# Optimization experiments

Hardware: AMD Instinct MI355X
Metric: run time of the kernel (lower is better)

## Reference

```python
import jax, jax.numpy as jnp
import numpy as np

D_MODEL = 1024
NUM_HEADS = 16
D_K = D_MODEL // NUM_HEADS


def setup_inputs() -> dict:
    key = jax.random.key(0)
    ks = jax.random.split(key, 9)
    B, S = 2, 2048
    s = 1.0 / np.sqrt(D_MODEL)
    inp = {
        "x": jax.random.normal(ks[0], (B, S, D_MODEL), dtype=jnp.float32),
        "Wq": jax.random.normal(ks[1], (D_MODEL, D_MODEL), dtype=jnp.float32) * s,
        "bq": jnp.zeros((D_MODEL,), dtype=jnp.float32),
        "Wk": jax.random.normal(ks[2], (D_MODEL, D_MODEL), dtype=jnp.float32) * s,
        "bk": jnp.zeros((D_MODEL,), dtype=jnp.float32),
        "Wv": jax.random.normal(ks[3], (D_MODEL, D_MODEL), dtype=jnp.float32) * s,
        "bv": jnp.zeros((D_MODEL,), dtype=jnp.float32),
        "Wo": jax.random.normal(ks[4], (D_MODEL, D_MODEL), dtype=jnp.float32) * s,
        "bo": jnpp if False else jnp.zeros((D_MODEL,), dtype=jnp.float32),
    }
    return inp


def reference(x, Wq, bq, Wk, bk, Wv, bv, Wo, bo):
    B, S, _ = x.shape
    H, Dk = NUM_HEADS, D_K

    def proj(W, b):
        # [B,S,D] -> [B,H,S,Dk]
        return (x @ W + b).reshape(B, S, H, Dk).transpose(0, 2, 1, 3)

    Q = proj(Wq, bq)
    K = proj(Wk, bk)
    V = proj(Wv, bv)

    scores = jnp.einsum("bhqd,bhkd->bhqk", Q, K) / np.sqrt(Dk)
    attn = jax.nn.softmax(scores, axis=-1)  # no mask, dropout p=0 (eval)
    out = jnp.einsum("bhqk,bhkd->bhqd", attn, V)
    out = out.transpose(0, 2, 1, 3).reshape(B, S, D_MODEL)
    return out @ Wo + bo
```

## Files before the change

kernel.cpp:

```cpp
#include <hip/hip_runtime.h>
#include <hip/hip_bf16.h>
#include <cstdint>
#include <math.h>

#define D_MODEL 1024
#define NHEADS  16
#define DK      64
#define BATCH   2
#define SEQ     2048
#define M_TOTAL (BATCH*SEQ)
#define NSPLIT  2
#define NTS     (SEQ/64/NSPLIT)

using f32x4  = __attribute__((ext_vector_type(4)))  float;
using f32x16 = __attribute__((ext_vector_type(16))) float;
using s16x8  = __attribute__((ext_vector_type(8)))  short;

#define CSC (0.125f * 1.44269504088896341f)

__device__ __forceinline__ unsigned short bf16r(float f) {
    __hip_bfloat16 h = __float2bfloat16(f);
    return *(unsigned short*)&h;
}
__device__ __forceinline__ uint32_t cvtpk(float lo, float hi) {
    uint32_t r;
    asm("v_cvt_pk_bf16_f32 %0, %1, %2" : "=v"(r) : "v"(lo), "v"(hi));
    return r;
}
__device__ __forceinline__ float b2f(unsigned short u) {
    uint32_t x = (uint32_t)u << 16;
    float f;
    __builtin_memcpy(&f, &x, 4);
    return f;
}

__global__ __launch_bounds__(256) void conv_all(const float* __restrict__ x,
                                                unsigned short* __restrict__ xb,
                                                const float* __restrict__ W0, const float* __restrict__ W1,
                                                const float* __restrict__ W2, const float* __restrict__ W3,
                                                unsigned short* __restrict__ T0, unsigned short* __restrict__ T1,
                                                unsigned short* __restrict__ T2, unsigned short* __restrict__ T3)
{
    __shared__ float tile[32][33];
    const int bid = blockIdx.x;
    const int t   = threadIdx.x;

    if (bid < 2048) {
        const size_t i = ((size_t)bid * 256 + t) * 8;
        const float4 a = *(const float4*)(x + i);
        const float4 b = *(const float4*)(x + i + 4);
        ushort4 r0, r1;
        r0.x = bf16r(a.x); r0.y = bf16r(a.y); r0.z = bf16r(a.z); r0.w = bf16r(a.w);
        r1.x = bf16r(b.x); r1.y = bf16r(b.y); r1.z = bf16r(b.z); r1.w = bf16r(b.w);
        *(ushort4*)(xb + i)     = r0;
        *(ushort4*)(xb + i + 4) = r1;
        return;
    }

    const int b2   = bid - 2048;
    const int z    = b2 >> 10;
    const int rest = b2 & 1023;
    const int kblk = rest & 31;
    const int nblk = rest >> 5;
    const float* W; unsigned short* T;
    switch (z) {
        case 0: W = W0; T = T0; break;
        case 1: W = W1; T = T1; break;
        case 2: W = W2; T = T2; break;
        default: W = W3; T = T3; break;
    }
    const int r  = t >> 3;
    const int c4 = (t & 7) * 4;
    const int k0 = kblk * 32;
    const int n0 = nblk * 32;

    const float4 v = *(const float4*)(W + (size_t)(k0 + r) * 1024 + n0 + c4);
    tile[r][c4 + 0] = v.x; tile[r][c4 + 1] = v.y; tile[r][c4 + 2] = v.z; tile[r][c4 + 3] = v.w;
    __syncthreads();
    ushort4 o;
    o.x = bf16r(tile[c4 + 0][r]);
    o.y = bf16r(tile[c4 + 1][r]);
    o.z = bf16r(tile[c4 + 2][r]);
    o.w = bf16r(tile[c4 + 3][r]);
    *(ushort4*)(T + (size_t)(n0 + r) * 1024 + k0 + c4) = o;
}

template<int OUT_BF16>
__device__ __forceinline__ void gemm_mfma_body(const unsigned short* __restrict__ A,
                                               const unsigned short* __restrict__ Bt,
                                               const float* __restrict__ bias,
                                               void* __restrict__ C,
                                               float oscale)
{
    __shared__ unsigned short As[128 * 64];
    __shared__ unsigned short Bs[128 * 64];

    const int t    = threadIdx.x;
    const int w    = t >> 6;
    const int lane = t & 63;
    const int ln   = lane & 15;
    const int g    = lane >> 4;
    const int wr   = w >> 1, wc = w & 1;
    const int m0   = blockIdx.y * 128;
    const int n0   = blockIdx.x * 128;

    f32x4 acc[4][4];
#pragma unroll
    for (int mi = 0; mi < 4; ++mi)
#pragma unroll
        for (int ni = 0; ni < 4; ++ni)
#pragma unroll
            for (int j = 0; j < 4; ++j) acc[mi][ni][j] = 0.f;

    const int lrow = lane >> 3;
    const int lchk = (lane & 7) ^ lrow;
    const unsigned short* Ag = A  + (size_t)(m0 + w * 32 + lrow) * 1024 + lchk * 8;
    const unsigned short* Bg = Bt + (size_t)(n0 + w * 32 + lrow) * 1024 + lchk * 8;

    for (int kt = 0; kt < 16; ++kt) {
        const int k0 = kt * 64;
#pragma unroll
        for (int i = 0; i < 4; ++i) {
            __builtin_amdgcn_global_load_lds(Ag + (size_t)i * 8 * 1024 + k0,
                                             &As[(w * 32 + i * 8) * 64], 16, 0, 0);
            __builtin_amdgcn_global_load_lds(Bg + (size_t)i * 8 * 1024 + k0,
                                             &Bs[(w * 32 + i * 8) * 64], 16, 0, 0);
        }
        __syncthreads();

#pragma unroll
        for (int ks = 0; ks < 2; ++ks) {
            s16x8 af[4], bf[4];
#pragma unroll
            for (int mi = 0; mi < 4; ++mi) {
                const int row = wr * 64 + mi * 16 + ln;
                af[mi] = *(const s16x8*)((const char*)As + row * 128 +
                                         (((ks * 4 + g) ^ (ln & 7)) * 16));
            }
#pragma unroll
            for (int ni = 0; ni < 4; ++ni) {
                const int row = wc * 64 + ni * 16 + ln;
                bf[ni] = *(const s16x8*)((const char*)Bs + row * 128 +
                                         (((ks * 4 + g) ^ (ln & 7)) * 16));
            }
#pragma unroll
            for (int mi = 0; mi < 4; ++mi)
#pragma unroll
                for (int ni = 0; ni < 4; ++ni)
                    acc[mi][ni] = __builtin_amdgcn_mfma_f32_16x16x32_bf16(
                        af[mi], bf[ni], acc[mi][ni], 0, 0, 0);
        }
        __syncthreads();
    }

#pragma unroll
    for (int ni = 0; ni < 4; ++ni) {
        const int n = n0 + wc * 64 + ni * 16 + ln;
        const float bn = bias[n];
#pragma unroll
        for (int mi = 0; mi < 4; ++mi) {
            const int m = m0 + wr * 64 + mi * 16 + g * 4;
#pragma unroll
            for (int j = 0; j < 4; ++j) {
                const float v = (acc[mi][ni][j] + bn) * oscale;
                if constexpr (OUT_BF16)
                    ((unsigned short*)C)[(size_t)(m + j) * 1024 + n] = bf16r(v);
                else
                    ((float*)C)[(size_t)(m + j) * 1024 + n] = v;
            }
        }
    }
}

__global__ __launch_bounds__(256) void qkv_mfma(const unsigned short* __restrict__ xb,
                                                const unsigned short* __restrict__ Wqt, const float* __restrict__ bq,
                                                const unsigned short* __restrict__ Wkt, const float* __restrict__ bk,
                                                const unsigned short* __restrict__ Wvt, const float* __restrict__ bv,
                                                unsigned short* __restrict__ Q,
                                                unsigned short* __restrict__ K,
                                                unsigned short* __restrict__ V)
{
    if (blockIdx.z == 0)      gemm_mfma_body<1>(xb, Wqt, bq, Q, CSC);
    else if (blockIdx.z == 1) gemm_mfma_body<1>(xb, Wkt, bk, K, 1.0f);
    else                      gemm_mfma_body<1>(xb, Wvt, bv, V, 1.0f);
}

__global__ __launch_bounds__(256) void oproj_mfma(const unsigned short* __restrict__ Ab,
                                                  const unsigned short* __restrict__ Wot,
                                                  const float* __restrict__ bo,
                                                  float* __restrict__ C)
{
    gemm_mfma_body<0>(Ab, Wot, bo, C, 1.0f);
}

__global__ __launch_bounds__(256, 4) void attn_mfma(const unsigned short* __restrict__ Qb,
                                                    const unsigned short* __restrict__ Kb,
                                                    const unsigned short* __restrict__ Vb,
                                                    unsigned short* __restrict__ O0,
                                                    unsigned short* __restrict__ O1,
                                                    float* __restrict__ lbuf)
{
    __shared__ unsigned short Klds[2][64 * 64];
    __shared__ unsigned short Vtlds[64 * 64];

    const int t   = threadIdx.x;
    const int wid = t >> 6;
    const int l   = t & 63;
    const int q32 = l & 31;
    const int hi  = l >> 5;

    const int bh = blockIdx.y;
    const int b  = bh >> 4;
    const int h  = bh & 15;
    const int sp = blockIdx.z;
    const int qbase = blockIdx.x * 128 + wid * 32;
    const size_t qrow = (size_t)(b * SEQ + qbase + q32);
    const size_t kv0  = (size_t)(b * SEQ) + (size_t)sp * (SEQ / NSPLIT);

    s16x8 qf[4];
    {
        const unsigned short* qp = Qb + qrow * D_MODEL + h * DK + 8 * hi;
#pragma unroll
        for (int ks = 0; ks < 4; ++ks) qf[ks] = *(const s16x8*)(qp + 16 * ks);
    }

    f32x16 ot0, ot1;
#pragma unroll
    for (int i = 0; i < 16; ++i) { ot0[i] = 0.f; ot1[i] = 0.f; }
    float lsum = 0.f;

    const unsigned short* Kgl = Kb + (kv0 + wid * 16 + (l >> 3)) * D_MODEL
                                   + h * DK + 8 * ((l & 7) ^ (l >> 3));
    auto stage_K = [&](int kt, int buf) {
        const size_t off = (size_t)kt * 64 * D_MODEL;
#pragma unroll
        for (int j = 0; j < 2; ++j)
            __builtin_amdgcn_global_load_lds(Kgl + off + (size_t)j * 8 * D_MODEL,
                                             &Klds[buf][(wid * 16 + j * 8) * 64],
                                             16, 0, 0);
    };

    const int vk2  = 2 * (t & 31);
    const int pk2  = (vk2 & ~12) | ((vk2 & 4) << 1) | ((vk2 & 8) >> 1);
    const int vd0  = 8 * (t >> 5);
    const unsigned short* Vg = Vb + (kv0 + vk2) * D_MODEL + h * DK + vd0;

    s16x8 vr0, vr1;
    auto load_V = [&](int kt) {
        const size_t off = (size_t)kt * 64 * D_MODEL;
        vr0 = *(const s16x8*)(Vg + off);
        vr1 = *(const s16x8*)(Vg + off + D_MODEL);
    };
    auto write_V = [&]() {
#pragma unroll
        for (int i = 0; i < 8; ++i) {
            const int d = vd0 + i;
            const uint32_t val = (uint32_t)(unsigned short)vr0[i] |
                                 ((uint32_t)(unsigned short)vr1[i] << 16);
            *(uint32_t*)((char*)Vtlds + d * 128 +
                         16 * ((pk2 >> 3) ^ (d & 7)) + (pk2 & 7) * 2) = val;
        }
    };

    stage_K(0, 0);
    load_V(0);
    write_V();
    __syncthreads();

    for (int kt = 0; kt < NTS; ++kt) {
        const int cur = kt & 1;
        if (kt < NTS - 1) { stage_K(kt + 1, cur ^ 1); load_V(kt + 1); }

        const char* Kl = (const char*)&Klds[cur][0];

        f32x16 s0, s1;
#pragma unroll
        for (int i = 0; i < 16; ++i) { s0[i] = 0.f; s1[i] = 0.f; }
        __builtin_amdgcn_s_setprio(1);
#pragma unroll
        for (int ks = 0; ks < 4; ++ks) {
            const int c = hi + 2 * ks;
            const s16x8 a0 = *(const s16x8*)(Kl + q32 * 128 + 16 * (c ^ (q32 & 7)));
            const s16x8 a1 = *(const s16x8*)(Kl + (q32 + 32) * 128 + 16 * (c ^ (q32 & 7)));
            s0 = __builtin_amdgcn_mfma_f32_32x32x16_bf16(a0, qf[ks], s0, 0, 0, 0);
            s1 = __builtin_amdgcn_mfma_f32_32x32x16_bf16(a1, qf[ks], s1, 0, 0, 0);
        }
        __builtin_amdgcn_s_setprio(0);

        float la = 0.f, lb = 0.f, lc = 0.f, ld = 0.f;
#pragma unroll
        for (int i = 0; i < 4; ++i) {
            s0[4 * i + 0] = exp2f(s0[4 * i + 0]); la += s0[4 * i + 0];
            s0[4 * i + 1] = exp2f(s0[4 * i + 1]); lb += s0[4 * i + 1];
            s0[4 * i + 2] = exp2f(s0[4 * i + 2]); lc += s0[4 * i + 2];
            s0[4 * i + 3] = exp2f(s0[4 * i + 3]); ld += s0[4 * i + 3];
            s1[4 * i + 0] = exp2f(s1[4 * i + 0]); la += s1[4 * i + 0];
            s1[4 * i + 1] = exp2f(s1[4 * i + 1]); lb += s1[4 * i + 1];
            s1[4 * i + 2] = exp2f(s1[4 * i + 2]); lc += s1[4 * i + 2];
            s1[4 * i + 3] = exp2f(s1[4 * i + 3]); ld += s1[4 * i + 3];
        }
        lsum += (la + lb) + (lc + ld);

        s16x8 pf[4];
        {
            union { uint32_t u[4]; s16x8 v; } F;
#pragma unroll
            for (int e = 0; e < 4; ++e) F.u[e] = cvtpk(s0[2 * e], s0[2 * e + 1]);
            pf[0] = F.v;
#pragma unroll
            for (int e = 0; e < 4; ++e) F.u[e] = cvtpk(s0[8 + 2 * e], s0[9 + 2 * e]);
            pf[1] = F.v;
#pragma unroll
            for (int e = 0; e < 4; ++e) F.u[e] = cvtpk(s1[2 * e], s1[2 * e + 1]);
            pf[2] = F.v;
#pragma unroll
            for (int e = 0; e < 4; ++e) F.u[e] = cvtpk(s1[8 + 2 * e], s1[9 + 2 * e]);
            pf[3] = F.v;
        }

        __builtin_amdgcn_s_setprio(1);
#pragma unroll
        for (int ks = 0; ks < 4; ++ks) {
            const int c = hi + 2 * ks;
            const s16x8 av0 = *(const s16x8*)((char*)Vtlds + q32 * 128 + 16 * (c ^ (q32 & 7)));
            const s16x8 av1 = *(const s16x8*)((char*)Vtlds + (q32 + 32) * 128 + 16 * (c ^ (q32 & 7)));
            ot0 = __builtin_amdgcn_mfma_f32_32x32x16_bf16(av0, pf[ks], ot0, 0, 0, 0);
            ot1 = __builtin_amdgcn_mfma_f32_32x32x16_bf16(av1, pf[ks], ot1, 0, 0, 0);
        }
        __builtin_amdgcn_s_setprio(0);

        __syncthreads();
        if (kt < NTS - 1) write_V();
        __syncthreads();
    }

    const float ltot = lsum + __shfl_xor(lsum, 32);
    const size_t prow = (size_t)bh * SEQ + qbase + q32;
    if (hi == 0)
        lbuf[(size_t)sp * (BATCH * NHEADS * SEQ) + prow] = ltot;

    unsigned short* op = ((sp == 0) ? O0 : O1) + prow * DK;
#pragma unroll
    for (int j = 0; j < 4; ++j) {
        uint2 st0, st1;
        st0.x = cvtpk(ot0[4 * j + 0], ot0[4 * j + 1]);
        st0.y = cvtpk(ot0[4 * j + 2], ot0[4 * j + 3]);
        st1.x = cvtpk(ot1[4 * j + 0], ot1[4 * j + 1]);
        st1.y = cvtpk(ot1[4 * j + 2], ot1[4 * j + 3]);
        *(uint2*)(op + 8 * j + 4 * hi)      = st0;
        *(uint2*)(op + 32 + 8 * j + 4 * hi) = st1;
    }
}

__global__ __launch_bounds__(256) void attn_combine(const unsigned short* __restrict__ O0,
                                                    const unsigned short* __restrict__ O1,
                                                    const float* __restrict__ lbuf,
                                                    unsigned short* __restrict__ Ab)
{
    const int tid = blockIdx.x * 256 + threadIdx.x;
    const int row = tid >> 3;
    const int d0  = (tid & 7) * 8;
    const size_t NROW = (size_t)BATCH * NHEADS * SEQ;

    const float rinv = 1.0f / (lbuf[row] + lbuf[NROW + row]);

    const size_t src = (size_t)row * DK + d0;
    const ushort4 a0 = *(const ushort4*)(O0 + src);
    const ushort4 a1 = *(const ushort4*)(O0 + src + 4);
    const ushort4 b0 = *(const ushort4*)(O1 + src);
    const ushort4 b1 = *(const ushort4*)(O1 + src + 4);

    const int bh = row >> 11, s = row & 2047;
    const int b = bh >> 4, h = bh & 15;
    unsigned short* dst = Ab + ((size_t)(b * SEQ + s)) * D_MODEL + h * DK + d0;

    ushort4 o0, o1;
    o0.x = bf16r((b2f(a0.x) + b2f(b0.x)) * rinv);
    o0.y = bf16r((b2f(a0.y) + b2f(b0.y)) * rinv);
    o0.z = bf16r((b2f(a0.z) + b2f(b0.z)) * rinv);
    o0.w = bf16r((b2f(a0.w) + b2f(b0.w)) * rinv);
    o1.x = bf16r((b2f(a1.x) + b2f(b1.x)) * rinv);
    o1.y = bf16r((b2f(a1.y) + b2f(b1.y)) * rinv);
    o1.z = bf16r((b2f(a1.z) + b2f(b1.z)) * rinv);
    o1.w = bf16r((b2f(a1.w) + b2f(b1.w)) * rinv);
    *(ushort4*)(dst)     = o0;
    *(ushort4*)(dst + 4) = o1;
}

extern "C" void kernel_launch(void* const* d_in, const int* in_sizes, int n_in,
                              void* d_out, int out_size, void* d_ws, size_t ws_size,
                              hipStream_t stream)
{
    const float* x  = (const float*)d_in[0];
    const float* Wq = (const float*)d_in[1];
    const float* bq = (const float*)d_in[2];
    const float* Wk = (const float*)d_in[3];
    const float* bk = (const float*)d_in[4];
    const float* Wv = (const float*)d_in[5];
    const float* bv = (const float*)d_in[6];
    const float* Wo = (const float*)d_in[7];
    const float* bo = (const float*)d_in[8];

    float* out = (float*)d_out;

    const size_t mat  = (size_t)M_TOTAL * D_MODEL;
    const size_t wmat = (size_t)D_MODEL * D_MODEL;
    unsigned short* xb  = (unsigned short*)d_ws;
    unsigned short* Wqt = xb  + mat;
    unsigned short* Wkt = Wqt + wmat;
    unsigned short* Wvt = Wkt + wmat;
    unsigned short* Wot = Wvt + wmat;
    unsigned short* Qb  = Wot + wmat;
    unsigned short* Kb  = Qb  + mat;
    unsigned short* Vb  = Kb  + mat;
    unsigned short* Ab  = Vb  + mat;
    unsigned short* Op0 = Ab  + mat;
    unsigned short* Op1 = Op0 + mat;
    float*          lbuf = (float*)xb;

    conv_all<<<dim3(6144), 256, 0, stream>>>(x, xb, Wq, Wk, Wv, Wo, Wqt, Wkt, Wvt, Wot);

    qkv_mfma<<<dim3(8, 32, 3), 256, 0, stream>>>(xb, Wqt, bq, Wkt, bk, Wvt, bv, Qb, Kb, Vb);

    attn_mfma<<<dim3(SEQ / 128, BATCH * NHEADS, NSPLIT), 256, 0, stream>>>(
        Qb, Kb, Vb, Op0, Op1, lbuf);

    attn_combine<<<dim3((BATCH * NHEADS * SEQ * 8) / 256), 256, 0, stream>>>(
        Op0, Op1, lbuf, Ab);

    oproj_mfma<<<dim3(8, 32), 256, 0, stream>>>(Ab, Wot, bo, out);
}
```

Measured before the change: 140.6 us.

## Stage K through registers into single LDS buffer and flatten attention grid

```diff
diff --git a/kernel.cpp b/kernel.cpp
--- a/kernel.cpp
+++ b/kernel.cpp
@@ -200,7 +200,7 @@
                                                     unsigned short* __restrict__ O1,
                                                     float* __restrict__ lbuf)
 {
-    __shared__ unsigned short Klds[2][64 * 64];
+    __shared__ unsigned short Klds [64 * 64];
     __shared__ unsigned short Vtlds[64 * 64];
 
     const int t   = threadIdx.x;
@@ -209,11 +209,14 @@
     const int q32 = l & 31;
     const int hi  = l >> 5;
 
-    const int bh = blockIdx.y;
-    const int b  = bh >> 4;
-    const int h  = bh & 15;
-    const int sp = blockIdx.z;
-    const int qbase = blockIdx.x * 128 + wid * 32;
+    const int bid = blockIdx.x;
+    const int grp = bid & 63;
+    const int qb  = bid >> 6;
+    const int bh  = grp >> 1;
+    const int sp  = grp & 1;
+    const int b   = bh >> 4;
+    const int h   = bh & 15;
+    const int qbase = qb * 128 + wid * 32;
     const size_t qrow = (size_t)(b * SEQ + qbase + q32);
     const size_t kv0  = (size_t)(b * SEQ) + (size_t)sp * (SEQ / NSPLIT);
 
@@ -229,29 +232,28 @@
     for (int i = 0; i < 16; ++i) { ot0[i] = 0.f; ot1[i] = 0.f; }
     float lsum = 0.f;
 
-    const unsigned short* Kgl = Kb + (kv0 + wid * 16 + (l >> 3)) * D_MODEL
-                                   + h * DK + 8 * ((l & 7) ^ (l >> 3));
-    auto stage_K = [&](int kt, int buf) {
-        const size_t off = (size_t)kt * 64 * D_MODEL;
-#pragma unroll
-        for (int j = 0; j < 2; ++j)
-            __builtin_amdgcn_global_load_lds(Kgl + off + (size_t)j * 8 * D_MODEL,
-                                             &Klds[buf][(wid * 16 + j * 8) * 64],
-                                             16, 0, 0);
-    };
-
+    const int skey = t >> 3;
+    const int sc8  = t & 7;
     const int vk2  = 2 * (t & 31);
     const int pk2  = (vk2 & ~12) | ((vk2 & 4) << 1) | ((vk2 & 8) >> 1);
     const int vd0  = 8 * (t >> 5);
+    const unsigned short* Kg = Kb + (kv0 + skey) * D_MODEL + h * DK + 8 * sc8;
     const unsigned short* Vg = Vb + (kv0 + vk2) * D_MODEL + h * DK + vd0;
-
-    s16x8 vr0, vr1;
-    auto load_V = [&](int kt) {
+    char* const kw0 = (char*)Klds + skey * 128        + 16 * (sc8 ^ (skey & 7));
+    char* const kw1 = (char*)Klds + (skey + 32) * 128 + 16 * (sc8 ^ (skey & 7));
+
+    s16x8 kr0, kr1, vr0, vr1;
+
+    auto load_regs = [&](int kt) {
         const size_t off = (size_t)kt * 64 * D_MODEL;
+        kr0 = *(const s16x8*)(Kg + off);
+        kr1 = *(const s16x8*)(Kg + off + (size_t)32 * D_MODEL);
         vr0 = *(const s16x8*)(Vg + off);
         vr1 = *(const s16x8*)(Vg + off + D_MODEL);
     };
-    auto write_V = [&]() {
+    auto write_stage = [&]() {
+        *(s16x8*)kw0 = kr0;
+        *(s16x8*)kw1 = kr1;
 #pragma unroll
         for (int i = 0; i < 8; ++i) {
             const int d = vd0 + i;
@@ -262,16 +264,12 @@
         }
     };
 
-    stage_K(0, 0);
-    load_V(0);
-    write_V();
+    load_regs(0);
+    write_stage();
     __syncthreads();
 
     for (int kt = 0; kt < NTS; ++kt) {
-        const int cur = kt & 1;
-        if (kt < NTS - 1) { stage_K(kt + 1, cur ^ 1); load_V(kt + 1); }
-
-        const char* Kl = (const char*)&Klds[cur][0];
+        if (kt < NTS - 1) load_regs(kt + 1);
 
         f32x16 s0, s1;
 #pragma unroll
@@ -280,8 +278,8 @@
 #pragma unroll
         for (int ks = 0; ks < 4; ++ks) {
             const int c = hi + 2 * ks;
-            const s16x8 a0 = *(const s16x8*)(Kl + q32 * 128 + 16 * (c ^ (q32 & 7)));
-            const s16x8 a1 = *(const s16x8*)(Kl + (q32 + 32) * 128 + 16 * (c ^ (q32 & 7)));
+            const s16x8 a0 = *(const s16x8*)((char*)Klds + q32 * 128 + 16 * (c ^ (q32 & 7)));
+            const s16x8 a1 = *(const s16x8*)((char*)Klds + (q32 + 32) * 128 + 16 * (c ^ (q32 & 7)));
             s0 = __builtin_amdgcn_mfma_f32_32x32x16_bf16(a0, qf[ks], s0, 0, 0, 0);
             s1 = __builtin_amdgcn_mfma_f32_32x32x16_bf16(a1, qf[ks], s1, 0, 0, 0);
         }
@@ -330,7 +328,7 @@
         __builtin_amdgcn_s_setprio(0);
 
         __syncthreads();
-        if (kt < NTS - 1) write_V();
+        if (kt < NTS - 1) write_stage();
         __syncthreads();
     }
 
@@ -422,7 +420,7 @@
 
     qkv_mfma<<<dim3(8, 32, 3), 256, 0, stream>>>(xb, Wqt, bq, Wkt, bk, Wvt, bv, Qb, Kb, Vb);
 
-    attn_mfma<<<dim3(SEQ / 128, BATCH * NHEADS, NSPLIT), 256, 0, stream>>>(
+    attn_mfma<<<dim3((SEQ / 128) * BATCH * NHEADS * NSPLIT), 256, 0, stream>>>(
         Qb, Kb, Vb, Op0, Op1, lbuf);
 
     attn_combine<<<dim3((BATCH * NHEADS * SEQ * 8) / 256), 256, 0, stream>>>(
```

New measurement: 139.0 us. Within noise of the previous version (-1.2%).
